# Optimization experiments

Hardware: AMD Instinct MI355X
Metric: run time of the kernel (lower is better)

## Reference

```python
import jax, jax.numpy as jnp
import numpy as np

N = 100000

def gcn_conv(x, src, dst, W, b, n):
    # x: [N, Fin]; src/dst: [E'] (self-loops already included); W: [Fin, Fout]
    h = x @ W  # [N, Fout]
    deg = jax.ops.segment_sum(jnp.ones_like(dst, dtype=h.dtype), dst, num_segments=n)  # [N]
    dinv = deg ** -0.5  # deg >= 1 due to self-loops
    norm = dinv[src] * dinv[dst]  # [E']
    msg = h[src] * norm[:, None]  # gather + scale, [E', Fout]
    out = jax.ops.segment_sum(msg, dst, num_segments=n)  # scatter-add to targets
    return out + b

def setup_inputs() -> dict:
    key = jax.random.key(0)
    k1, k2, k3, k4, k5, k6 = jax.random.split(key, 6)
    x = jax.random.normal(k1, (N, 128), dtype=jnp.float32)
    edge_index = jax.random.randint(k2, (2, 1600000), 0, N, dtype=jnp.int32)
    W1 = jax.random.normal(k3, (128, 64), dtype=jnp.float32) * 0.1
    b1 = jnp.zeros((64,), dtype=jnp.float32)
    W2 = jax.random.normal(k4, (64, 41), dtype=jnp.float32) * 0.1
    b2 = jnp.zeros((41,), dtype=jnp.float32)
    return {"x": x, "edge_index": edge_index, "W1": W1, "b1": b1, "W2": W2, "b2": b2}

def reference(x, edge_index, W1, b1, W2, b2):
    n = x.shape[0]
    loops = jnp.arange(n, dtype=edge_index.dtype)
    src = jnp.concatenate([edge_index[0], loops])  # add self-loops (PyG gcn_norm default)
    dst = jnp.concatenate([edge_index[1], loops])
    # dropout is identity in eval mode (self.training=False)
    h = gcn_conv(x, src, dst, W1, b1, n)
    h = jax.nn.relu(h)
    out = gcn_conv(h, src, dst, W2, b2, n)
    return out
```

## Files before the change

### kernel.cpp

```cpp
#include <hip/hip_runtime.h>


#define FIN 128
#define F1  64
#define F2  41
#define FP  64

#define BSH    8
#define BCAP   6144
#define NBMAX  512
#define CHUNK_P 4096

#define MT 128
#define KC 16

__device__ __forceinline__ unsigned short f2bf(float f) {
    unsigned u = __builtin_bit_cast(unsigned, f);
    u += 0x7FFFu + ((u >> 16) & 1u);
    return (unsigned short)(u >> 16);
}
__device__ __forceinline__ float bf2f(unsigned short h) {
    unsigned u = ((unsigned)h) << 16;
    return __builtin_bit_cast(float, u);
}

__global__ void k_zero(int* __restrict__ p, int n) {
    int i = blockIdx.x * blockDim.x + threadIdx.x;
    if (i < n) p[i] = 0;
}

__global__ __launch_bounds__(256) void k_part(
    const int* __restrict__ src, const int* __restrict__ dst,
    int* __restrict__ gcur, int* __restrict__ pairs, int E) {
    __shared__ int hist[NBMAX];
    __shared__ int gsh[NBMAX];
    __shared__ int lex[256];
    __shared__ int limg[CHUNK_P];
    __shared__ int lsh[CHUNK_P];
    __shared__ int stot;
    int tid = threadIdx.x;
    int e0  = blockIdx.x * CHUNK_P;
    hist[tid] = 0; hist[tid + 256] = 0;
    __syncthreads();
    for (int j = 0; j < CHUNK_P / 256; j++) {
        int e = e0 + j * 256 + tid;
        if (e < E) atomicAdd(&hist[dst[e] >> BSH], 1);
    }
    __syncthreads();
    int b0 = 2 * tid, b1 = 2 * tid + 1;
    int c0 = hist[b0], c1 = hist[b1];
    int s  = c0 + c1;
    lex[tid] = s;
    __syncthreads();
    for (int off = 1; off < 256; off <<= 1) {
        int v = lex[tid];
        int a = (tid >= off) ? lex[tid - off] : 0;
        __syncthreads();
        lex[tid] = v + a;
        __syncthreads();
    }
    int incl = lex[tid];
    if (tid == 255) stot = incl;
    int ex = incl - s;
    int l0 = ex, l1 = ex + c0;
    int g0 = c0 ? atomicAdd(&gcur[b0], c0) : 0;
    int g1 = c1 ? atomicAdd(&gcur[b1], c1) : 0;
    hist[b0] = l0; hist[b1] = l1;
    gsh[b0]  = b0 * BCAP + g0 - l0;
    gsh[b1]  = b1 * BCAP + g1 - l1;
    __syncthreads();
    for (int j = 0; j < CHUNK_P / 256; j++) {
        int e = e0 + j * 256 + tid;
        if (e < E) {
            int d = dst[e], sv = src[e];
            int b = d >> BSH;
            int p = atomicAdd(&hist[b], 1);
            limg[p] = (sv << BSH) | (d & 255);
            lsh[p]  = gsh[b];
        }
    }
    __syncthreads();
    int tot = stot;
    for (int k = tid; k < tot; k += 256)
        pairs[k + lsh[k]] = limg[k];
}

__global__ __launch_bounds__(256) void k_build(
    const int* __restrict__ gcur, const int* __restrict__ pairs,
    int* __restrict__ adjcur, int* __restrict__ adj,
    int2* __restrict__ rowinfo, float* __restrict__ dinv, int n) {
    __shared__ int lcnt[256];
    __shared__ int lex[256];
    __shared__ int lcur[256];
    __shared__ int ladj[BCAP];
    __shared__ int sbase;
    int tid = threadIdx.x;
    int b   = blockIdx.x;
    int cntb  = gcur[b]; if (cntb > BCAP) cntb = BCAP;
    int node0 = b << BSH;
    const int* pb = pairs + (size_t)b * BCAP;

    if (tid == 0) sbase = atomicAdd(adjcur, cntb);
    lcnt[tid] = 0;
    __syncthreads();
    for (int k = tid; k < cntb; k += 256) atomicAdd(&lcnt[pb[k] & 255], 1);
    __syncthreads();
    int own = lcnt[tid];
    lex[tid] = own;
    __syncthreads();
    for (int off = 1; off < 256; off <<= 1) {
        int val = lex[tid];
        int add = (tid >= off) ? lex[tid - off] : 0;
        __syncthreads();
        lex[tid] = val + add;
        __syncthreads();
    }
    int excl = lex[tid] - own;
    __syncthreads();
    lex[tid]  = excl;
    lcur[tid] = excl;
    __syncthreads();
    for (int k = tid; k < cntb; k += 256) {
        int pk  = pb[k];
        int pos = atomicAdd(&lcur[pk & 255], 1);
        ladj[pos] = pk >> BSH;
    }
    __syncthreads();
    {
        int s0 = excl;
        for (int i = 1; i < own; i++) {
            int key = ladj[s0 + i];
            int j = i - 1;
            while (j >= 0 && ladj[s0 + j] > key) {
                ladj[s0 + j + 1] = ladj[s0 + j];
                j--;
            }
            ladj[s0 + j + 1] = key;
        }
    }
    __syncthreads();
    int base = sbase;
    for (int k = tid; k < cntb; k += 256) adj[base + k] = ladj[k];
    int node = node0 + tid;
    if (node < n) {
        rowinfo[node] = make_int2(base + excl, own);
        dinv[node]    = rsqrtf((float)own + 1.0f);
    }
}

__global__ __launch_bounds__(256) void k_mm1(
    const float* __restrict__ x, const float* __restrict__ W1,
    const float* __restrict__ dinv, unsigned short* __restrict__ hs, int n) {
    __shared__ float Ws[FIN * F1];
    __shared__ float As[KC][MT];
    int t  = threadIdx.x;
    int n0 = blockIdx.x * MT;
#pragma unroll
    for (int j = 0; j < 8; j++) {
        int f = j * 256 + t;
        ((float4*)Ws)[f] = ((const float4*)W1)[f];
    }
    int m0 = (t & 15) * 8;
    int c0 = (t >> 4) * 4;
    int m_l = t & 127;
    int kh  = (t >> 7) * 8;
    bool mvalid = (n0 + m_l) < n;
    const float* xrow = x + (size_t)(n0 + m_l) * FIN + kh;
    float acc[8][4] = {};
    for (int kc = 0; kc < FIN; kc += KC) {
        __syncthreads();
        float4 v0 = mvalid ? *(const float4*)(xrow + kc)     : float4{0.f,0.f,0.f,0.f};
        float4 v1 = mvalid ? *(const float4*)(xrow + kc + 4) : float4{0.f,0.f,0.f,0.f};
        As[kh + 0][m_l] = v0.x; As[kh + 1][m_l] = v0.y;
        As[kh + 2][m_l] = v0.z; As[kh + 3][m_l] = v0.w;
        As[kh + 4][m_l] = v1.x; As[kh + 5][m_l] = v1.y;
        As[kh + 6][m_l] = v1.z; As[kh + 7][m_l] = v1.w;
        __syncthreads();
#pragma unroll
        for (int k = 0; k < KC; k++) {
            float4 a0 = *(const float4*)&As[k][m0];
            float4 a1 = *(const float4*)&As[k][m0 + 4];
            float4 w  = *(const float4*)&Ws[(kc + k) * F1 + c0];
            float a[8] = {a0.x, a0.y, a0.z, a0.w, a1.x, a1.y, a1.z, a1.w};
#pragma unroll
            for (int i = 0; i < 8; i++) {
                acc[i][0] += a[i] * w.x;
                acc[i][1] += a[i] * w.y;
                acc[i][2] += a[i] * w.z;
                acc[i][3] += a[i] * w.w;
            }
        }
    }
#pragma unroll
    for (int i = 0; i < 8; i++) {
        int node = n0 + m0 + i;
        if (node < n) {
            float dv = dinv[node];
            ushort4 o = { f2bf(acc[i][0] * dv), f2bf(acc[i][1] * dv),
                          f2bf(acc[i][2] * dv), f2bf(acc[i][3] * dv) };
            *(ushort4*)&hs[((size_t)node << 6) + c0] = o;
        }
    }
}

__global__ __launch_bounds__(256) void k_agg1(
    const int2* __restrict__ rowinfo, const int* __restrict__ adj,
    const unsigned short* __restrict__ hs, const float* __restrict__ dinv,
    const float* __restrict__ b1, unsigned short* __restrict__ h1b, int n, int E) {
    int node = blockIdx.x * 4 + (threadIdx.x >> 6);
    if (node >= n) return;
    int lane = threadIdx.x & 63;
    int grp  = lane >> 4;
    int p4   = (lane & 15) * 4;
    int2 ri = rowinfo[node];
    int beg = ri.x, deg = ri.y;
    float4 acc = {0.f, 0.f, 0.f, 0.f};
    if (grp == 0) {
        ushort4 u = *(const ushort4*)&hs[((size_t)node << 6) + p4];
        acc.x = bf2f(u.x); acc.y = bf2f(u.y); acc.z = bf2f(u.z); acc.w = bf2f(u.w);
    }
    for (int base = 0; base < deg; base += 64) {
        int m = deg - base; if (m > 64) m = 64;
        int idx = beg + base + lane;
        int myoff = adj[idx < E ? idx : 0] << 6;
        int e = 0;
        for (; e + 16 <= m; e += 16) {
            int o0 = __shfl(myoff, e + grp),      o1 = __shfl(myoff, e + 4 + grp);
            int o2 = __shfl(myoff, e + 8 + grp),  o3 = __shfl(myoff, e + 12 + grp);
            ushort4 u0 = *(const ushort4*)&hs[(size_t)o0 + p4];
            ushort4 u1 = *(const ushort4*)&hs[(size_t)o1 + p4];
            ushort4 u2 = *(const ushort4*)&hs[(size_t)o2 + p4];
            ushort4 u3 = *(const ushort4*)&hs[(size_t)o3 + p4];
            acc.x += (bf2f(u0.x) + bf2f(u1.x)) + (bf2f(u2.x) + bf2f(u3.x));
            acc.y += (bf2f(u0.y) + bf2f(u1.y)) + (bf2f(u2.y) + bf2f(u3.y));
            acc.z += (bf2f(u0.z) + bf2f(u1.z)) + (bf2f(u2.z) + bf2f(u3.z));
            acc.w += (bf2f(u0.w) + bf2f(u1.w)) + (bf2f(u2.w) + bf2f(u3.w));
        }
        for (; e < m; e += 4) {
            int sl = e + grp;
            int o = __shfl(myoff, sl);
            if (sl < m) {
                ushort4 u = *(const ushort4*)&hs[(size_t)o + p4];
                acc.x += bf2f(u.x); acc.y += bf2f(u.y);
                acc.z += bf2f(u.z); acc.w += bf2f(u.w);
            }
        }
    }
    acc.x += __shfl_xor(acc.x, 16); acc.y += __shfl_xor(acc.y, 16);
    acc.z += __shfl_xor(acc.z, 16); acc.w += __shfl_xor(acc.w, 16);
    acc.x += __shfl_xor(acc.x, 32); acc.y += __shfl_xor(acc.y, 32);
    acc.z += __shfl_xor(acc.z, 32); acc.w += __shfl_xor(acc.w, 32);
    if (grp == 0) {
        float dv = dinv[node];
        float4 bg = *(const float4*)&b1[p4];
        float vx = acc.x * dv + bg.x; vx = vx > 0.f ? vx : 0.f;
        float vy = acc.y * dv + bg.y; vy = vy > 0.f ? vy : 0.f;
        float vz = acc.z * dv + bg.z; vz = vz > 0.f ? vz : 0.f;
        float vw = acc.w * dv + bg.w; vw = vw > 0.f ? vw : 0.f;
        ushort4 o = { f2bf(vx), f2bf(vy), f2bf(vz), f2bf(vw) };
        *(ushort4*)&h1b[((size_t)node << 6) + p4] = o;
    }
}

__global__ __launch_bounds__(256) void k_mm2(
    const unsigned short* __restrict__ h1b, const float* __restrict__ W2,
    const float* __restrict__ dinv, unsigned short* __restrict__ hs2, int n) {
    __shared__ float Ws[F1 * FP];
    __shared__ float As[KC][MT];
    int t  = threadIdx.x;
    int n0 = blockIdx.x * MT;
    for (int idx = t; idx < F1 * FP; idx += 256) {
        int k = idx >> 6, c = idx & 63;
        Ws[idx] = (c < F2) ? W2[k * F2 + c] : 0.f;
    }
    int m0 = (t & 15) * 8;
    int c0 = (t >> 4) * 4;
    int m_l = t & 127;
    int kh  = (t >> 7) * 8;
    bool mvalid = (n0 + m_l) < n;
    const unsigned short* hrow = h1b + ((size_t)(n0 + m_l) << 6) + kh;
    float acc[8][4] = {};
    for (int kc = 0; kc < F1; kc += KC) {
        __syncthreads();
        ushort4 u0 = mvalid ? *(const ushort4*)(hrow + kc)     : ushort4{0,0,0,0};
        ushort4 u1 = mvalid ? *(const ushort4*)(hrow + kc + 4) : ushort4{0,0,0,0};
        As[kh + 0][m_l] = bf2f(u0.x); As[kh + 1][m_l] = bf2f(u0.y);
        As[kh + 2][m_l] = bf2f(u0.z); As[kh + 3][m_l] = bf2f(u0.w);
        As[kh + 4][m_l] = bf2f(u1.x); As[kh + 5][m_l] = bf2f(u1.y);
        As[kh + 6][m_l] = bf2f(u1.z); As[kh + 7][m_l] = bf2f(u1.w);
        __syncthreads();
#pragma unroll
        for (int k = 0; k < KC; k++) {
            float4 a0 = *(const float4*)&As[k][m0];
            float4 a1 = *(const float4*)&As[k][m0 + 4];
            float4 w  = *(const float4*)&Ws[(kc + k) * FP + c0];
            float a[8] = {a0.x, a0.y, a0.z, a0.w, a1.x, a1.y, a1.z, a1.w};
#pragma unroll
            for (int i = 0; i < 8; i++) {
                acc[i][0] += a[i] * w.x;
                acc[i][1] += a[i] * w.y;
                acc[i][2] += a[i] * w.z;
                acc[i][3] += a[i] * w.w;
            }
        }
    }
#pragma unroll
    for (int i = 0; i < 8; i++) {
        int node = n0 + m0 + i;
        if (node < n) {
            float dv = dinv[node];
            ushort4 o = { f2bf(acc[i][0] * dv), f2bf(acc[i][1] * dv),
                          f2bf(acc[i][2] * dv), f2bf(acc[i][3] * dv) };
            *(ushort4*)&hs2[((size_t)node << 6) + c0] = o;
        }
    }
}

__global__ __launch_bounds__(256) void k_agg2(
    const int2* __restrict__ rowinfo, const int* __restrict__ adj,
    const unsigned short* __restrict__ hs2, const float* __restrict__ dinv,
    const float* __restrict__ b2, float* __restrict__ out, int n, int E) {
    int node = blockIdx.x * 4 + (threadIdx.x >> 6);
    if (node >= n) return;
    int lane = threadIdx.x & 63;
    int grp  = lane >> 4;
    int p4   = (lane & 15) * 4;
    int2 ri = rowinfo[node];
    int beg = ri.x, deg = ri.y;
    float4 acc = {0.f, 0.f, 0.f, 0.f};
    if (grp == 0) {
        ushort4 u = *(const ushort4*)&hs2[((size_t)node << 6) + p4];
        acc.x = bf2f(u.x); acc.y = bf2f(u.y); acc.z = bf2f(u.z); acc.w = bf2f(u.w);
    }
    for (int base = 0; base < deg; base += 64) {
        int m = deg - base; if (m > 64) m = 64;
        int idx = beg + base + lane;
        int myoff = adj[idx < E ? idx : 0] << 6;
        int e = 0;
        for (; e + 16 <= m; e += 16) {
            int o0 = __shfl(myoff, e + grp),      o1 = __shfl(myoff, e + 4 + grp);
            int o2 = __shfl(myoff, e + 8 + grp),  o3 = __shfl(myoff, e + 12 + grp);
            ushort4 u0 = *(const ushort4*)&hs2[(size_t)o0 + p4];
            ushort4 u1 = *(const ushort4*)&hs2[(size_t)o1 + p4];
            ushort4 u2 = *(const ushort4*)&hs2[(size_t)o2 + p4];
            ushort4 u3 = *(const ushort4*)&hs2[(size_t)o3 + p4];
            acc.x += (bf2f(u0.x) + bf2f(u1.x)) + (bf2f(u2.x) + bf2f(u3.x));
            acc.y += (bf2f(u0.y) + bf2f(u1.y)) + (bf2f(u2.y) + bf2f(u3.y));
            acc.z += (bf2f(u0.z) + bf2f(u1.z)) + (bf2f(u2.z) + bf2f(u3.z));
            acc.w += (bf2f(u0.w) + bf2f(u1.w)) + (bf2f(u2.w) + bf2f(u3.w));
        }
        for (; e < m; e += 4) {
            int sl = e + grp;
            int o = __shfl(myoff, sl);
            if (sl < m) {
                ushort4 u = *(const ushort4*)&hs2[(size_t)o + p4];
                acc.x += bf2f(u.x); acc.y += bf2f(u.y);
                acc.z += bf2f(u.z); acc.w += bf2f(u.w);
            }
        }
    }
    acc.x += __shfl_xor(acc.x, 16); acc.y += __shfl_xor(acc.y, 16);
    acc.z += __shfl_xor(acc.z, 16); acc.w += __shfl_xor(acc.w, 16);
    acc.x += __shfl_xor(acc.x, 32); acc.y += __shfl_xor(acc.y, 32);
    acc.z += __shfl_xor(acc.z, 32); acc.w += __shfl_xor(acc.w, 32);
    if (grp == 0) {
        float dv = dinv[node];
        float vv[4] = {acc.x, acc.y, acc.z, acc.w};
#pragma unroll
        for (int j = 0; j < 4; j++) {
            int f = p4 + j;
            if (f < F2) out[(size_t)node * F2 + f] = vv[j] * dv + b2[f];
        }
    }
}

extern "C" void kernel_launch(void* const* d_in, const int* in_sizes, int n_in,
                              void* d_out, int out_size, void* d_ws, size_t ws_size,
                              hipStream_t stream) {
    const float* x  = (const float*)d_in[0];
    const int*   ei = (const int*)d_in[1];
    const float* W1 = (const float*)d_in[2];
    const float* b1 = (const float*)d_in[3];
    const float* W2 = (const float*)d_in[4];
    const float* b2 = (const float*)d_in[5];
    float* out = (float*)d_out;

    const int n = in_sizes[0] / FIN;
    const int E = in_sizes[1] / 2;
    const int* src = ei;
    const int* dst = ei + E;
    const int nbuck   = (n + 255) >> BSH;
    const int nchunks = (E + CHUNK_P - 1) / CHUNK_P;
    const int nmm     = (n + MT - 1) / MT;
    const int nagg    = (n + 3) / 4;

    char* ws = (char*)d_ws;
    size_t off = 0;
    auto alloc = [&](size_t bytes) {
        void* p = ws + off;
        off = (off + bytes + 511) & ~(size_t)511;
        return p;
    };
    int*   gcur    = (int*)alloc((size_t)(NBMAX + 1) * 4);
    int*   pairs   = (int*)alloc((size_t)nbuck * BCAP * 4);
    int*   adj     = (int*)alloc((size_t)E * 4);
    int2*  rowinfo = (int2*)alloc((size_t)n * 8);
    float* dinv    = (float*)alloc((size_t)n * 4);
    unsigned short* hs1 = (unsigned short*)alloc((size_t)n * FP * 2);
    unsigned short* hs2 = (unsigned short*)alloc((size_t)n * FP * 2);
    unsigned short* h1b = (unsigned short*)alloc((size_t)n * FP * 2);

    k_zero<<<(NBMAX + 256) / 256, 256, 0, stream>>>(gcur, NBMAX + 1);
    k_part<<<nchunks, 256, 0, stream>>>(src, dst, gcur, pairs, E);
    k_build<<<nbuck, 256, 0, stream>>>(gcur, pairs, gcur + NBMAX, adj, rowinfo, dinv, n);
    k_mm1<<<nmm, 256, 0, stream>>>(x, W1, dinv, hs1, n);
    k_agg1<<<nagg, 256, 0, stream>>>(rowinfo, adj, hs1, dinv, b1, h1b, n, E);
    k_mm2<<<nmm, 256, 0, stream>>>(h1b, W2, dinv, hs2, n);
    k_agg2<<<nagg, 256, 0, stream>>>(rowinfo, adj, hs2, dinv, b2, out, n, E);
}
```

Measured before the change: 336.0 us.

## Fuse edge partitioning with first matmul and move source scaling into aggregation

The edge-partition kernel and the first dense matmul become one launch, with blocks split by index so both run concurrently. The matmul no longer needs dinv, so the source-side normalization moves into agg1 as a per-edge dinv gather broadcast via shuffles. The partition kernel now preloads src/dst into registers, and the per-row insertion sort of adjacency lists in k_build is removed. The costs are extra per-edge dinv loads and multiplies in agg1, non-deterministic neighbor order (so float summation order varies), and higher register and shared memory use in the fused kernel.

```diff
diff --git a/kernel.cpp b/kernel.cpp
--- a/kernel.cpp
+++ b/kernel.cpp
@@ -29,60 +29,118 @@
     if (i < n) p[i] = 0;
 }
 
-__global__ __launch_bounds__(256) void k_part(
+__global__ __launch_bounds__(256) void k_partmm1(
     const int* __restrict__ src, const int* __restrict__ dst,
-    int* __restrict__ gcur, int* __restrict__ pairs, int E) {
-    __shared__ int hist[NBMAX];
-    __shared__ int gsh[NBMAX];
-    __shared__ int lex[256];
-    __shared__ int limg[CHUNK_P];
-    __shared__ int lsh[CHUNK_P];
-    __shared__ int stot;
+    int* __restrict__ gcur, int* __restrict__ pairs, int E, int nchunks,
+    const float* __restrict__ x, const float* __restrict__ W1,
+    unsigned short* __restrict__ hs, int n) {
+    __shared__ alignas(16) char smem[40960];
     int tid = threadIdx.x;
-    int e0  = blockIdx.x * CHUNK_P;
-    hist[tid] = 0; hist[tid + 256] = 0;
-    __syncthreads();
-    for (int j = 0; j < CHUNK_P / 256; j++) {
-        int e = e0 + j * 256 + tid;
-        if (e < E) atomicAdd(&hist[dst[e] >> BSH], 1);
-    }
-    __syncthreads();
-    int b0 = 2 * tid, b1 = 2 * tid + 1;
-    int c0 = hist[b0], c1 = hist[b1];
-    int s  = c0 + c1;
-    lex[tid] = s;
-    __syncthreads();
-    for (int off = 1; off < 256; off <<= 1) {
-        int v = lex[tid];
-        int a = (tid >= off) ? lex[tid - off] : 0;
-        __syncthreads();
-        lex[tid] = v + a;
-        __syncthreads();
-    }
-    int incl = lex[tid];
-    if (tid == 255) stot = incl;
-    int ex = incl - s;
-    int l0 = ex, l1 = ex + c0;
-    int g0 = c0 ? atomicAdd(&gcur[b0], c0) : 0;
-    int g1 = c1 ? atomicAdd(&gcur[b1], c1) : 0;
-    hist[b0] = l0; hist[b1] = l1;
-    gsh[b0]  = b0 * BCAP + g0 - l0;
-    gsh[b1]  = b1 * BCAP + g1 - l1;
-    __syncthreads();
-    for (int j = 0; j < CHUNK_P / 256; j++) {
-        int e = e0 + j * 256 + tid;
-        if (e < E) {
-            int d = dst[e], sv = src[e];
-            int b = d >> BSH;
-            int p = atomicAdd(&hist[b], 1);
-            limg[p] = (sv << BSH) | (d & 255);
-            lsh[p]  = gsh[b];
-        }
-    }
-    __syncthreads();
-    int tot = stot;
-    for (int k = tid; k < tot; k += 256)
-        pairs[k + lsh[k]] = limg[k];
+    if ((int)blockIdx.x < nchunks) {
+        int* hist = (int*)smem;
+        int* gsh  = hist + NBMAX;
+        int* lex  = gsh + NBMAX;
+        int* stot = lex + 256;
+        int* limg = stot + 1;
+        int* lsh  = limg + CHUNK_P;
+        int e0  = blockIdx.x * CHUNK_P;
+        int ds[CHUNK_P / 256], ss[CHUNK_P / 256];
+#pragma unroll
+        for (int j = 0; j < CHUNK_P / 256; j++) {
+            int e = e0 + j * 256 + tid;
+            if (e < E) { ds[j] = dst[e]; ss[j] = src[e]; } else ds[j] = -1;
+        }
+        hist[tid] = 0; hist[tid + 256] = 0;
+        __syncthreads();
+#pragma unroll
+        for (int j = 0; j < CHUNK_P / 256; j++)
+            if (ds[j] >= 0) atomicAdd(&hist[ds[j] >> BSH], 1);
+        __syncthreads();
+        int b0 = 2 * tid, b1 = 2 * tid + 1;
+        int c0 = hist[b0], c1 = hist[b1];
+        int s  = c0 + c1;
+        lex[tid] = s;
+        __syncthreads();
+        for (int off = 1; off < 256; off <<= 1) {
+            int v = lex[tid];
+            int a = (tid >= off) ? lex[tid - off] : 0;
+            __syncthreads();
+            lex[tid] = v + a;
+            __syncthreads();
+        }
+        int incl = lex[tid];
+        if (tid == 255) stot[0] = incl;
+        int ex = incl - s;
+        int l0 = ex, l1 = ex + c0;
+        int g0 = c0 ? atomicAdd(&gcur[b0], c0) : 0;
+        int g1 = c1 ? atomicAdd(&gcur[b1], c1) : 0;
+        hist[b0] = l0; hist[b1] = l1;
+        gsh[b0]  = b0 * BCAP + g0 - l0;
+        gsh[b1]  = b1 * BCAP + g1 - l1;
+        __syncthreads();
+#pragma unroll
+        for (int j = 0; j < CHUNK_P / 256; j++) {
+            if (ds[j] >= 0) {
+                int b = ds[j] >> BSH;
+                int p = atomicAdd(&hist[b], 1);
+                limg[p] = (ss[j] << BSH) | (ds[j] & 255);
+                lsh[p]  = gsh[b];
+            }
+        }
+        __syncthreads();
+        int tot = stot[0];
+        for (int k = tid; k < tot; k += 256)
+            pairs[k + lsh[k]] = limg[k];
+    } else {
+        float* Ws = (float*)smem;
+        float (*As)[MT] = (float(*)[MT])(smem + FIN * F1 * 4);
+        int n0 = ((int)blockIdx.x - nchunks) * MT;
+#pragma unroll
+        for (int j = 0; j < 8; j++) {
+            int f = j * 256 + tid;
+            ((float4*)Ws)[f] = ((const float4*)W1)[f];
+        }
+        int m0 = (tid & 15) * 8;
+        int c0 = (tid >> 4) * 4;
+        int m_l = tid & 127;
+        int kh  = (tid >> 7) * 8;
+        bool mvalid = (n0 + m_l) < n;
+        const float* xrow = x + (size_t)(n0 + m_l) * FIN + kh;
+        float acc[8][4] = {};
+        for (int kc = 0; kc < FIN; kc += KC) {
+            __syncthreads();
+            float4 v0 = mvalid ? *(const float4*)(xrow + kc)     : float4{0.f,0.f,0.f,0.f};
+            float4 v1 = mvalid ? *(const float4*)(xrow + kc + 4) : float4{0.f,0.f,0.f,0.f};
+            As[kh + 0][m_l] = v0.x; As[kh + 1][m_l] = v0.y;
+            As[kh + 2][m_l] = v0.z; As[kh + 3][m_l] = v0.w;
+            As[kh + 4][m_l] = v1.x; As[kh + 5][m_l] = v1.y;
+            As[kh + 6][m_l] = v1.z; As[kh + 7][m_l] = v1.w;
+            __syncthreads();
+#pragma unroll
+            for (int k = 0; k < KC; k++) {
+                float4 a0 = *(const float4*)&As[k][m0];
+                float4 a1 = *(const float4*)&As[k][m0 + 4];
+                float4 w  = *(const float4*)&Ws[(kc + k) * F1 + c0];
+                float a[8] = {a0.x, a0.y, a0.z, a0.w, a1.x, a1.y, a1.z, a1.w};
+#pragma unroll
+                for (int i = 0; i < 8; i++) {
+                    acc[i][0] += a[i] * w.x;
+                    acc[i][1] += a[i] * w.y;
+                    acc[i][2] += a[i] * w.z;
+                    acc[i][3] += a[i] * w.w;
+                }
+            }
+        }
+#pragma unroll
+        for (int i = 0; i < 8; i++) {
+            int node = n0 + m0 + i;
+            if (node < n) {
+                ushort4 o = { f2bf(acc[i][0]), f2bf(acc[i][1]),
+                              f2bf(acc[i][2]), f2bf(acc[i][3]) };
+                *(ushort4*)&hs[((size_t)node << 6) + c0] = o;
+            }
+        }
+    }
 }
 
 __global__ __launch_bounds__(256) void k_build(
@@ -126,80 +184,12 @@
         ladj[pos] = pk >> BSH;
     }
     __syncthreads();
-    {
-        int s0 = excl;
-        for (int i = 1; i < own; i++) {
-            int key = ladj[s0 + i];
-            int j = i - 1;
-            while (j >= 0 && ladj[s0 + j] > key) {
-                ladj[s0 + j + 1] = ladj[s0 + j];
-                j--;
-            }
-            ladj[s0 + j + 1] = key;
-        }
-    }
-    __syncthreads();
     int base = sbase;
     for (int k = tid; k < cntb; k += 256) adj[base + k] = ladj[k];
     int node = node0 + tid;
     if (node < n) {
         rowinfo[node] = make_int2(base + excl, own);
         dinv[node]    = rsqrtf((float)own + 1.0f);
-    }
-}
-
-__global__ __launch_bounds__(256) void k_mm1(
-    const float* __restrict__ x, const float* __restrict__ W1,
-    const float* __restrict__ dinv, unsigned short* __restrict__ hs, int n) {
-    __shared__ float Ws[FIN * F1];
-    __shared__ float As[KC][MT];
-    int t  = threadIdx.x;
-    int n0 = blockIdx.x * MT;
-#pragma unroll
-    for (int j = 0; j < 8; j++) {
-        int f = j * 256 + t;
-        ((float4*)Ws)[f] = ((const float4*)W1)[f];
-    }
-    int m0 = (t & 15) * 8;
-    int c0 = (t >> 4) * 4;
-    int m_l = t & 127;
-    int kh  = (t >> 7) * 8;
-    bool mvalid = (n0 + m_l) < n;
-    const float* xrow = x + (size_t)(n0 + m_l) * FIN + kh;
-    float acc[8][4] = {};
-    for (int kc = 0; kc < FIN; kc += KC) {
-        __syncthreads();
-        float4 v0 = mvalid ? *(const float4*)(xrow + kc)     : float4{0.f,0.f,0.f,0.f};
-        float4 v1 = mvalid ? *(const float4*)(xrow + kc + 4) : float4{0.f,0.f,0.f,0.f};
-        As[kh + 0][m_l] = v0.x; As[kh + 1][m_l] = v0.y;
-        As[kh + 2][m_l] = v0.z; As[kh + 3][m_l] = v0.w;
-        As[kh + 4][m_l] = v1.x; As[kh + 5][m_l] = v1.y;
-        As[kh + 6][m_l] = v1.z; As[kh + 7][m_l] = v1.w;
-        __syncthreads();
-#pragma unroll
-        for (int k = 0; k < KC; k++) {
-            float4 a0 = *(const float4*)&As[k][m0];
-            float4 a1 = *(const float4*)&As[k][m0 + 4];
-            float4 w  = *(const float4*)&Ws[(kc + k) * F1 + c0];
-            float a[8] = {a0.x, a0.y, a0.z, a0.w, a1.x, a1.y, a1.z, a1.w};
-#pragma unroll
-            for (int i = 0; i < 8; i++) {
-                acc[i][0] += a[i] * w.x;
-                acc[i][1] += a[i] * w.y;
-                acc[i][2] += a[i] * w.z;
-                acc[i][3] += a[i] * w.w;
-            }
-        }
-    }
-#pragma unroll
-    for (int i = 0; i < 8; i++) {
-        int node = n0 + m0 + i;
-        if (node < n) {
-            float dv = dinv[node];
-            ushort4 o = { f2bf(acc[i][0] * dv), f2bf(acc[i][1] * dv),
-                          f2bf(acc[i][2] * dv), f2bf(acc[i][3] * dv) };
-            *(ushort4*)&hs[((size_t)node << 6) + c0] = o;
-        }
     }
 }
 
@@ -214,35 +204,42 @@
     int p4   = (lane & 15) * 4;
     int2 ri = rowinfo[node];
     int beg = ri.x, deg = ri.y;
+    float dvn = dinv[node];
     float4 acc = {0.f, 0.f, 0.f, 0.f};
     if (grp == 0) {
         ushort4 u = *(const ushort4*)&hs[((size_t)node << 6) + p4];
-        acc.x = bf2f(u.x); acc.y = bf2f(u.y); acc.z = bf2f(u.z); acc.w = bf2f(u.w);
+        acc.x = dvn * bf2f(u.x); acc.y = dvn * bf2f(u.y);
+        acc.z = dvn * bf2f(u.z); acc.w = dvn * bf2f(u.w);
     }
     for (int base = 0; base < deg; base += 64) {
         int m = deg - base; if (m > 64) m = 64;
         int idx = beg + base + lane;
-        int myoff = adj[idx < E ? idx : 0] << 6;
+        int sidx  = adj[idx < E ? idx : 0];
+        float mydv = dinv[sidx];
+        int myoff  = sidx << 6;
         int e = 0;
         for (; e + 16 <= m; e += 16) {
             int o0 = __shfl(myoff, e + grp),      o1 = __shfl(myoff, e + 4 + grp);
             int o2 = __shfl(myoff, e + 8 + grp),  o3 = __shfl(myoff, e + 12 + grp);
+            float d0 = __shfl(mydv, e + grp),     d1 = __shfl(mydv, e + 4 + grp);
+            float d2 = __shfl(mydv, e + 8 + grp), d3 = __shfl(mydv, e + 12 + grp);
             ushort4 u0 = *(const ushort4*)&hs[(size_t)o0 + p4];
             ushort4 u1 = *(const ushort4*)&hs[(size_t)o1 + p4];
             ushort4 u2 = *(const ushort4*)&hs[(size_t)o2 + p4];
             ushort4 u3 = *(const ushort4*)&hs[(size_t)o3 + p4];
-            acc.x += (bf2f(u0.x) + bf2f(u1.x)) + (bf2f(u2.x) + bf2f(u3.x));
-            acc.y += (bf2f(u0.y) + bf2f(u1.y)) + (bf2f(u2.y) + bf2f(u3.y));
-            acc.z += (bf2f(u0.z) + bf2f(u1.z)) + (bf2f(u2.z) + bf2f(u3.z));
-            acc.w += (bf2f(u0.w) + bf2f(u1.w)) + (bf2f(u2.w) + bf2f(u3.w));
+            acc.x += d0*bf2f(u0.x) + d1*bf2f(u1.x) + d2*bf2f(u2.x) + d3*bf2f(u3.x);
+            acc.y += d0*bf2f(u0.y) + d1*bf2f(u1.y) + d2*bf2f(u2.y) + d3*bf2f(u3.y);
+            acc.z += d0*bf2f(u0.z) + d1*bf2f(u1.z) + d2*bf2f(u2.z) + d3*bf2f(u3.z);
+            acc.w += d0*bf2f(u0.w) + d1*bf2f(u1.w) + d2*bf2f(u2.w) + d3*bf2f(u3.w);
         }
         for (; e < m; e += 4) {
             int sl = e + grp;
             int o = __shfl(myoff, sl);
+            float d = __shfl(mydv, sl);
             if (sl < m) {
                 ushort4 u = *(const ushort4*)&hs[(size_t)o + p4];
-                acc.x += bf2f(u.x); acc.y += bf2f(u.y);
-                acc.z += bf2f(u.z); acc.w += bf2f(u.w);
+                acc.x += d * bf2f(u.x); acc.y += d * bf2f(u.y);
+                acc.z += d * bf2f(u.z); acc.w += d * bf2f(u.w);
             }
         }
     }
@@ -251,12 +248,11 @@
     acc.x += __shfl_xor(acc.x, 32); acc.y += __shfl_xor(acc.y, 32);
     acc.z += __shfl_xor(acc.z, 32); acc.w += __shfl_xor(acc.w, 32);
     if (grp == 0) {
-        float dv = dinv[node];
         float4 bg = *(const float4*)&b1[p4];
-        float vx = acc.x * dv + bg.x; vx = vx > 0.f ? vx : 0.f;
-        float vy = acc.y * dv + bg.y; vy = vy > 0.f ? vy : 0.f;
-        float vz = acc.z * dv + bg.z; vz = vz > 0.f ? vz : 0.f;
-        float vw = acc.w * dv + bg.w; vw = vw > 0.f ? vw : 0.f;
+        float vx = acc.x * dvn + bg.x; vx = vx > 0.f ? vx : 0.f;
+        float vy = acc.y * dvn + bg.y; vy = vy > 0.f ? vy : 0.f;
+        float vz = acc.z * dvn + bg.z; vz = vz > 0.f ? vz : 0.f;
+        float vw = acc.w * dvn + bg.w; vw = vw > 0.f ? vw : 0.f;
         ushort4 o = { f2bf(vx), f2bf(vy), f2bf(vz), f2bf(vw) };
         *(ushort4*)&h1b[((size_t)node << 6) + p4] = o;
     }
@@ -411,9 +407,9 @@
     unsigned short* h1b = (unsigned short*)alloc((size_t)n * FP * 2);
 
     k_zero<<<(NBMAX + 256) / 256, 256, 0, stream>>>(gcur, NBMAX + 1);
-    k_part<<<nchunks, 256, 0, stream>>>(src, dst, gcur, pairs, E);
+    k_partmm1<<<nchunks + nmm, 256, 0, stream>>>(src, dst, gcur, pairs, E, nchunks,
+                                                 x, W1, hs1, n);
     k_build<<<nbuck, 256, 0, stream>>>(gcur, pairs, gcur + NBMAX, adj, rowinfo, dinv, n);
-    k_mm1<<<nmm, 256, 0, stream>>>(x, W1, dinv, hs1, n);
     k_agg1<<<nagg, 256, 0, stream>>>(rowinfo, adj, hs1, dinv, b1, h1b, n, E);
     k_mm2<<<nmm, 256, 0, stream>>>(h1b, W2, dinv, hs2, n);
     k_agg2<<<nagg, 256, 0, stream>>>(rowinfo, adj, hs2, dinv, b2, out, n, E);
```

Result: faster. 286.3 us (-14.8%).
